# Optimization experiments

Hardware: AMD Instinct MI355X
Metric: run time of the kernel (lower is better)

The kernel has to match this reference:

```python
import jax, jax.numpy as jnp
import numpy as np

D = 1024
H = 16
HD = D // H


def setup_inputs() -> dict:
    key = jax.random.key(0)
    ks = jax.random.split(key, 9)
    s = 1.0 / np.sqrt(D)
    inp = {
        "x": jax.random.normal(ks[0], (2, 2048, D), dtype=jnp.float32),
        "Wq": jax.random.uniform(ks[1], (D, D), jnp.float32, -s, s),
        "bq": jax.random.uniform(ks[2], (D,), jnp.float32, -s, s),
        "Wk": jax.random.uniform(ks[3], (D, D), jnp.float32, -s, s),
        "bk": jax.random.uniform(ks[4], (D,), jnp.float32, -s, s),
        "Wv": jax.random.uniform(ks[5], (D, D), jnp.float32, -s, s),
        "bv": jax.random.uniform(ks[6], (D,), jnp.float32, -s, s),
        "Wo": jax.random.uniform(ks[7], (D, D), jnp.float32, -s, s),
        "bo": jax.random.uniform(ks[8], (D,), jnp.float32, -s, s),
    }
    return inp


def reference(x, Wq, bq, Wk, bk, Wv, bv, Wo, bo):
    B, S, _ = x.shape
    scale = jnp.sqrt(jnp.asarray(HD, dtype=jnp.float32))
    # QKV projections, split into heads: [B, H, S, HD]
    def proj(W, b):
        y = jnp.einsum('bsd,de->bse', x, W) + b
        return y.reshape(B, S, H, HD).transpose(0, 2, 1, 3)
    Q, K, V = proj(Wq, bq), proj(Wk, bk), proj(Wv, bv)
    scores = jnp.einsum('bhqd,bhkd->bhqk', Q, K) / scale  # [B,H,S,S]
    attn = jax.nn.softmax(scores, axis=-1)
    ctx = jnp.einsum('bhqk,bhkd->bhqd', attn, V)
    ctx = ctx.transpose(0, 2, 1, 3).reshape(B, S, D)
    return jnp.einsum('bsd,de->bse', ctx, Wo) + bo
```

## Files before the change

### kernel.cpp

```cpp
#include <hip/hip_runtime.h>
#include <hip/hip_bf16.h>

typedef __attribute__((ext_vector_type(8))) _Float16 f16x8;
typedef __attribute__((ext_vector_type(4))) float f32x4;

constexpr int Sc  = 2048;
constexpr int Dc  = 1024;
constexpr int Hc  = 16;
constexpr int HDc = 64;
constexpr int Mc  = 4096;

constexpr float ECs = 0.18033688011112042f;

__device__ __forceinline__ ushort f2h(float f) {
  return __builtin_bit_cast(ushort, (_Float16)f);
}

union US8 {
  ushort u[8];
  uint   w[4];
  f16x8  v;
};

__global__ __launch_bounds__(256) void split_x_kernel(
    const float* __restrict__ X, ushort* __restrict__ H) {
  const int i    = blockIdx.x * 256 + threadIdx.x;
  const float4 v = ((const float4*)X)[i];
  ushort4 h;
  h.x = f2h(v.x);
  h.y = f2h(v.y);
  h.z = f2h(v.z);
  h.w = f2h(v.w);
  ((ushort4*)H)[i] = h;
}

struct SplitP {
  const float* W[4];
  ushort*      Th[4];
};

__global__ __launch_bounds__(256) void split_wt_kernel(SplitP p) {
  __shared__ float T[64][69];
  const int z = blockIdx.z;
  const float* W = p.W[z];
  const int t  = threadIdx.x;
  const int c  = (t & 15) * 4;
  const int r  = t >> 4;
  const int n0 = blockIdx.x * 64, k0 = blockIdx.y * 64;
#pragma unroll
  for (int pp = 0; pp < 4; ++pp) {
    const int k    = r + pp * 16;
    const float4 v = *(const float4*)(W + (size_t)(k0 + k) * 1024 + n0 + c);
    T[k][c + 0] = v.x;
    T[k][c + 1] = v.y;
    T[k][c + 2] = v.z;
    T[k][c + 3] = v.w;
  }
  __syncthreads();
#pragma unroll
  for (int pp = 0; pp < 4; ++pp) {
    const int n = r + pp * 16;
    ushort4 h;
    h.x = f2h(T[c + 0][n]);
    h.y = f2h(T[c + 1][n]);
    h.z = f2h(T[c + 2][n]);
    h.w = f2h(T[c + 3][n]);
    *(ushort4*)(p.Th[z] + (size_t)(n0 + n) * 1024 + k0 + c) = h;
  }
}

struct GemmP {
  const ushort* Bh[3];
  const float*  bias[3];
  void*         Out[3];
};

template <bool QKV>
__global__ __launch_bounds__(256) void gemm_f16(
    const ushort* __restrict__ A, GemmP p) {
  __shared__ __align__(16) ushort As[128 * 32];
  __shared__ __align__(16) ushort Bs[128 * 32];

  const int t  = threadIdx.x;
  const int z  = blockIdx.z;
  const int m0 = blockIdx.x * 128, n0 = blockIdx.y * 128;
  const ushort* Bh  = p.Bh[z];
  const float* bias = p.bias[z];

  const int lane = t & 63, wave = t >> 6;
  const int wm = (wave & 1) * 64, wn = (wave >> 1) * 64;

  f32x4 acc[4][4];
#pragma unroll
  for (int i = 0; i < 4; ++i)
#pragma unroll
    for (int j = 0; j < 4; ++j) acc[i][j] = (f32x4){0.f, 0.f, 0.f, 0.f};

  const int am = t >> 2;
  const int ac = t & 3;
  const ushort* gA  = A  + (size_t)(m0 + am) * 1024 + ac * 8;
  const ushort* gBh = Bh + (size_t)(n0 + am) * 1024 + ac * 8;
  const int sw = ((ac + (am >> 1)) & 3) * 8;
  const int l0 = am * 32 + sw, l1 = (am + 64) * 32 + sw;

  const int fr  = lane & 15;
  const int fkb = (((lane >> 4) + (fr >> 1)) & 3) * 16;

  f16x8 rA0, rA1, rH0, rH1;
  rA0 = *(const f16x8*)(gA);
  rA1 = *(const f16x8*)(gA + 64 * 1024);
  rH0 = *(const f16x8*)(gBh);
  rH1 = *(const f16x8*)(gBh + 64 * 1024);

  for (int k0 = 0; k0 < 1024; k0 += 32) {
    __syncthreads();
    *(f16x8*)&As[l0] = rA0;
    *(f16x8*)&As[l1] = rA1;
    *(f16x8*)&Bs[l0] = rH0;
    *(f16x8*)&Bs[l1] = rH1;
    __syncthreads();

    if (k0 + 32 < 1024) {
      const int kn = k0 + 32;
      rA0 = *(const f16x8*)(gA + kn);
      rA1 = *(const f16x8*)(gA + kn + 64 * 1024);
      rH0 = *(const f16x8*)(gBh + kn);
      rH1 = *(const f16x8*)(gBh + kn + 64 * 1024);
    }

    f16x8 a[4], b_h[4];
#pragma unroll
    for (int i = 0; i < 4; ++i) {
      const int ra = (wm + i * 16 + fr) * 64 + fkb;
      const int rb = (wn + i * 16 + fr) * 64 + fkb;
      a[i]   = *(const f16x8*)((const char*)As + ra);
      b_h[i] = *(const f16x8*)((const char*)Bs + rb);
    }
#pragma unroll
    for (int i = 0; i < 4; ++i)
#pragma unroll
      for (int j = 0; j < 4; ++j)
        acc[i][j] = __builtin_amdgcn_mfma_f32_16x16x32_f16(a[i], b_h[j], acc[i][j], 0, 0, 0);
  }

  const float osc = (QKV && z == 0) ? ECs : 1.0f;
  const int cr = (lane >> 4) * 4;
  const int cc = lane & 15;
#pragma unroll
  for (int j = 0; j < 4; ++j) {
    const int n    = n0 + wn + j * 16 + cc;
    const float bv = bias[n];
#pragma unroll
    for (int i = 0; i < 4; ++i) {
      const int mb = m0 + wm + i * 16 + cr;
#pragma unroll
      for (int r = 0; r < 4; ++r) {
        const int m   = mb + r;
        const float v = (acc[i][j][r] + bv) * osc;
        if (QKV) {
          const int b = m >> 11, s = m & 2047, h = n >> 6, hd = n & 63;
          ((ushort*)p.Out[z])[(((size_t)(b * Hc + h) * Sc + s) << 6) + hd] = f2h(v);
        } else {
          ((float*)p.Out[z])[(size_t)m * 1024 + n] = v;
        }
      }
    }
  }
}

__global__ __launch_bounds__(256) void attn_mfma3(
    const ushort* __restrict__ Q, const ushort* __restrict__ K,
    const ushort* __restrict__ V, ushort* __restrict__ CTX) {
  __shared__ __align__(16) ushort Ks[64 * 72];
  __shared__ __align__(16) ushort Vt[64 * 72];

  const int t    = threadIdx.x;
  const int lane = t & 63, wave = t >> 6;
  const int c16 = lane & 15, quad = lane >> 4;
  const int bh = blockIdx.x, qt = blockIdx.y;
  const int bb = bh >> 4, hh = bh & 15;

  const ushort* Qb = Q + (size_t)bh * Sc * HDc + (size_t)qt * 128 * HDc;
  const ushort* Kb = K + (size_t)bh * Sc * HDc;
  const ushort* Vb = V + (size_t)bh * Sc * HDc;

  f16x8 aq[2][2];
#pragma unroll
  for (int mt = 0; mt < 2; ++mt)
#pragma unroll
    for (int c = 0; c < 2; ++c)
      aq[mt][c] = *(const f16x8*)(Qb + (size_t)(wave * 32 + mt * 16 + c16) * 64 + c * 32 + quad * 8);

  US8 ones_u;
#pragma unroll
  for (int e = 0; e < 8; ++e) ones_u.u[e] = 0x3C00;
  const f16x8 ones = ones_u.v;

  f32x4 ctx[2][4], lacc[2];
#pragma unroll
  for (int mt = 0; mt < 2; ++mt) {
    lacc[mt] = (f32x4){0.f, 0.f, 0.f, 0.f};
#pragma unroll
    for (int j = 0; j < 4; ++j) ctx[mt][j] = (f32x4){0.f, 0.f, 0.f, 0.f};
  }

  const int krow = t >> 2, kc = (t & 3) * 8;
  const int kg = t & 15, dg = t >> 4;
  const int lb = ((kg >> 3) << 5) | ((kg & 3) << 3) | (((kg >> 2) & 1) << 2);

  const ushort* gK = Kb + (size_t)krow * 64 + kc;
  const ushort* gV = Vb + (size_t)(kg * 4) * 64 + dg * 4;

  f16x8 kr0, kr1;
  ushort4 vr[4];
  kr0 = *(const f16x8*)(gK);
  kr1 = *(const f16x8*)(gK + 32);
#pragma unroll
  for (int i = 0; i < 4; ++i) vr[i] = *(const ushort4*)(gV + (size_t)i * 64);

  for (int kt = 0; kt < 32; ++kt) {
    __syncthreads();
    *(f16x8*)&Ks[krow * 72 + kc]      = kr0;
    *(f16x8*)&Ks[krow * 72 + kc + 32] = kr1;
    {
      const uint* w0 = (const uint*)&vr[0];
      const uint* w1 = (const uint*)&vr[1];
      const uint* w2 = (const uint*)&vr[2];
      const uint* w3 = (const uint*)&vr[3];
#pragma unroll
      for (int j = 0; j < 4; ++j) {
        const int  wd  = j >> 1;
        const uint sel = (j & 1) ? 0x07060302u : 0x05040100u;
        const uint lo  = __builtin_amdgcn_perm(w1[wd], w0[wd], sel);
        const uint hi  = __builtin_amdgcn_perm(w3[wd], w2[wd], sel);
        *(uint2*)&Vt[(dg * 4 + j) * 72 + lb] = make_uint2(lo, hi);
      }
    }
    __syncthreads();

    if (kt < 31) {
      const size_t adv = (size_t)(kt + 1) * 64 * 64;
      kr0 = *(const f16x8*)(gK + adv);
      kr1 = *(const f16x8*)(gK + adv + 32);
#pragma unroll
      for (int i = 0; i < 4; ++i) vr[i] = *(const ushort4*)(gV + adv + (size_t)i * 64);
    }

    f32x4 st[2][4];
#pragma unroll
    for (int mt = 0; mt < 2; ++mt)
#pragma unroll
      for (int j = 0; j < 4; ++j) st[mt][j] = (f32x4){0.f, 0.f, 0.f, 0.f};
#pragma unroll
    for (int c = 0; c < 2; ++c)
#pragma unroll
      for (int j = 0; j < 4; ++j) {
        const f16x8 ak = *(const f16x8*)&Ks[(j * 16 + c16) * 72 + c * 32 + quad * 8];
        st[0][j] = __builtin_amdgcn_mfma_f32_16x16x32_f16(ak, aq[0][c], st[0][j], 0, 0, 0);
        st[1][j] = __builtin_amdgcn_mfma_f32_16x16x32_f16(ak, aq[1][c], st[1][j], 0, 0, 0);
      }

    US8 pf[2][2];
#pragma unroll
    for (int mt = 0; mt < 2; ++mt)
#pragma unroll
      for (int c2 = 0; c2 < 2; ++c2)
#pragma unroll
        for (int w = 0; w < 4; ++w) {
          const int jj = c2 * 2 + (w >> 1);
          const int r0 = (w & 1) * 2;
          const float pe = __builtin_amdgcn_exp2f(st[mt][jj][r0]);
          const float po = __builtin_amdgcn_exp2f(st[mt][jj][r0 + 1]);
          const auto pk = __builtin_amdgcn_cvt_pkrtz(pe, po);
          pf[mt][c2].w[w] = __builtin_bit_cast(uint, pk);
        }

#pragma unroll
    for (int c2 = 0; c2 < 2; ++c2) {
      lacc[0] = __builtin_amdgcn_mfma_f32_16x16x32_f16(pf[0][c2].v, ones, lacc[0], 0, 0, 0);
      lacc[1] = __builtin_amdgcn_mfma_f32_16x16x32_f16(pf[1][c2].v, ones, lacc[1], 0, 0, 0);
#pragma unroll
      for (int j = 0; j < 4; ++j) {
        const f16x8 bv = *(const f16x8*)&Vt[(j * 16 + c16) * 72 + c2 * 32 + quad * 8];
        ctx[0][j] = __builtin_amdgcn_mfma_f32_16x16x32_f16(pf[0][c2].v, bv, ctx[0][j], 0, 0, 0);
        ctx[1][j] = __builtin_amdgcn_mfma_f32_16x16x32_f16(pf[1][c2].v, bv, ctx[1][j], 0, 0, 0);
      }
    }
  }

#pragma unroll
  for (int mt = 0; mt < 2; ++mt) {
#pragma unroll
    for (int r = 0; r < 4; ++r) {
      const float inv = 1.f / lacc[mt][r];
      const int srow  = qt * 128 + wave * 32 + mt * 16 + quad * 4 + r;
      const size_t rb = ((size_t)(bb * Sc + srow)) * 1024 + hh * 64;
#pragma unroll
      for (int j = 0; j < 4; ++j)
        CTX[rb + j * 16 + c16] = f2h(ctx[mt][j][r] * inv);
    }
  }
}

extern "C" void kernel_launch(void* const* d_in, const int* in_sizes, int n_in,
                              void* d_out, int out_size, void* d_ws, size_t ws_size,
                              hipStream_t stream) {
  (void)in_sizes; (void)n_in; (void)out_size; (void)ws_size;
  const float* x  = (const float*)d_in[0];
  const float* Wq = (const float*)d_in[1];
  const float* bq = (const float*)d_in[2];
  const float* Wk = (const float*)d_in[3];
  const float* bk = (const float*)d_in[4];
  const float* Wv = (const float*)d_in[5];
  const float* bv = (const float*)d_in[6];
  const float* Wo = (const float*)d_in[7];
  const float* bo = (const float*)d_in[8];

  const size_t MB = 1024 * 1024;
  char* w    = (char*)d_ws;
  ushort* Qw = (ushort*)(w + 0 * MB);
  ushort* Kw = (ushort*)(w + 8 * MB);
  ushort* Vw = (ushort*)(w + 16 * MB);
  ushort* Cw = (ushort*)(w + 24 * MB);
  ushort* Xh = (ushort*)(w + 32 * MB);
  ushort* WT = (ushort*)(w + 40 * MB);
  ushort* Whq = WT + 0 * 1048576;
  ushort* Whk = WT + 1 * 1048576;
  ushort* Whv = WT + 2 * 1048576;
  ushort* Who = WT + 3 * 1048576;

  const dim3 blk(256);

  split_x_kernel<<<4096, blk, 0, stream>>>(x, Xh);

  SplitP sp;
  sp.W[0] = Wq; sp.W[1] = Wk; sp.W[2] = Wv; sp.W[3] = Wo;
  sp.Th[0] = Whq; sp.Th[1] = Whk; sp.Th[2] = Whv; sp.Th[3] = Who;
  split_wt_kernel<<<dim3(16, 16, 4), blk, 0, stream>>>(sp);

  GemmP pq;
  pq.Bh[0] = Whq; pq.Bh[1] = Whk; pq.Bh[2] = Whv;
  pq.bias[0] = bq; pq.bias[1] = bk; pq.bias[2] = bv;
  pq.Out[0] = Qw; pq.Out[1] = Kw; pq.Out[2] = Vw;
  gemm_f16<true><<<dim3(Mc / 128, Dc / 128, 3), blk, 0, stream>>>(Xh, pq);

  attn_mfma3<<<dim3(2 * Hc, Sc / 128), blk, 0, stream>>>(Qw, Kw, Vw, Cw);

  GemmP po;
  po.Bh[0] = po.Bh[1] = po.Bh[2] = Who;
  po.bias[0] = po.bias[1] = po.bias[2] = bo;
  po.Out[0] = po.Out[1] = po.Out[2] = d_out;
  gemm_f16<false><<<dim3(Mc / 128, Dc / 128, 1), blk, 0, stream>>>(Cw, po);
}
```

Baseline: 199.2 us.

## Split attention key range across two blocks and add a combine kernel

The attention grid gains a z dimension that splits the 2048 keys into two halves. Each block writes an unnormalized fp16 partial context and its row sums to workspace, and a new combine kernel adds the two partials and normalizes them. The goal is to double the block count so the 512-block grid fills the GPU better. The cost is an extra launch, extra global traffic for the partials, and fp16 rounding of the unnormalized sums. The score MFMA chain is also restructured to start from a zero constant instead of zeroing the accumulators.

```diff
diff --git a/kernel.cpp b/kernel.cpp
--- a/kernel.cpp
+++ b/kernel.cpp
@@ -170,19 +170,20 @@
 
 __global__ __launch_bounds__(256) void attn_mfma3(
     const ushort* __restrict__ Q, const ushort* __restrict__ K,
-    const ushort* __restrict__ V, ushort* __restrict__ CTX) {
+    const ushort* __restrict__ V, ushort* __restrict__ CTXP,
+    float* __restrict__ LACC) {
   __shared__ __align__(16) ushort Ks[64 * 72];
   __shared__ __align__(16) ushort Vt[64 * 72];
 
   const int t    = threadIdx.x;
   const int lane = t & 63, wave = t >> 6;
   const int c16 = lane & 15, quad = lane >> 4;
-  const int bh = blockIdx.x, qt = blockIdx.y;
+  const int bh = blockIdx.x, qt = blockIdx.y, z = blockIdx.z;
   const int bb = bh >> 4, hh = bh & 15;
 
   const ushort* Qb = Q + (size_t)bh * Sc * HDc + (size_t)qt * 128 * HDc;
-  const ushort* Kb = K + (size_t)bh * Sc * HDc;
-  const ushort* Vb = V + (size_t)bh * Sc * HDc;
+  const ushort* Kb = K + (size_t)bh * Sc * HDc + (size_t)z * 16 * 64 * HDc;
+  const ushort* Vb = V + (size_t)bh * Sc * HDc + (size_t)z * 16 * 64 * HDc;
 
   f16x8 aq[2][2];
 #pragma unroll
@@ -195,6 +196,7 @@
 #pragma unroll
   for (int e = 0; e < 8; ++e) ones_u.u[e] = 0x3C00;
   const f16x8 ones = ones_u.v;
+  const f32x4 kZ = (f32x4){0.f, 0.f, 0.f, 0.f};
 
   f32x4 ctx[2][4], lacc[2];
 #pragma unroll
@@ -218,7 +220,7 @@
 #pragma unroll
   for (int i = 0; i < 4; ++i) vr[i] = *(const ushort4*)(gV + (size_t)i * 64);
 
-  for (int kt = 0; kt < 32; ++kt) {
+  for (int kt = 0; kt < 16; ++kt) {
     __syncthreads();
     *(f16x8*)&Ks[krow * 72 + kc]      = kr0;
     *(f16x8*)&Ks[krow * 72 + kc + 32] = kr1;
@@ -238,7 +240,7 @@
     }
     __syncthreads();
 
-    if (kt < 31) {
+    if (kt < 15) {
       const size_t adv = (size_t)(kt + 1) * 64 * 64;
       kr0 = *(const f16x8*)(gK + adv);
       kr1 = *(const f16x8*)(gK + adv + 32);
@@ -248,17 +250,17 @@
 
     f32x4 st[2][4];
 #pragma unroll
-    for (int mt = 0; mt < 2; ++mt)
-#pragma unroll
-      for (int j = 0; j < 4; ++j) st[mt][j] = (f32x4){0.f, 0.f, 0.f, 0.f};
-#pragma unroll
-    for (int c = 0; c < 2; ++c)
-#pragma unroll
-      for (int j = 0; j < 4; ++j) {
-        const f16x8 ak = *(const f16x8*)&Ks[(j * 16 + c16) * 72 + c * 32 + quad * 8];
-        st[0][j] = __builtin_amdgcn_mfma_f32_16x16x32_f16(ak, aq[0][c], st[0][j], 0, 0, 0);
-        st[1][j] = __builtin_amdgcn_mfma_f32_16x16x32_f16(ak, aq[1][c], st[1][j], 0, 0, 0);
-      }
+    for (int j = 0; j < 4; ++j) {
+      const f16x8 ak0 = *(const f16x8*)&Ks[(j * 16 + c16) * 72 + quad * 8];
+      st[0][j] = __builtin_amdgcn_mfma_f32_16x16x32_f16(ak0, aq[0][0], kZ, 0, 0, 0);
+      st[1][j] = __builtin_amdgcn_mfma_f32_16x16x32_f16(ak0, aq[1][0], kZ, 0, 0, 0);
+    }
+#pragma unroll
+    for (int j = 0; j < 4; ++j) {
+      const f16x8 ak1 = *(const f16x8*)&Ks[(j * 16 + c16) * 72 + 32 + quad * 8];
+      st[0][j] = __builtin_amdgcn_mfma_f32_16x16x32_f16(ak1, aq[0][1], st[0][j], 0, 0, 0);
+      st[1][j] = __builtin_amdgcn_mfma_f32_16x16x32_f16(ak1, aq[1][1], st[1][j], 0, 0, 0);
+    }
 
     US8 pf[2][2];
 #pragma unroll
@@ -288,18 +290,40 @@
     }
   }
 
+  ushort* Cp = CTXP + (size_t)z * Mc * 1024;
+  float*  Lp = LACC + (size_t)z * 2 * Hc * Sc;
 #pragma unroll
   for (int mt = 0; mt < 2; ++mt) {
 #pragma unroll
     for (int r = 0; r < 4; ++r) {
-      const float inv = 1.f / lacc[mt][r];
       const int srow  = qt * 128 + wave * 32 + mt * 16 + quad * 4 + r;
       const size_t rb = ((size_t)(bb * Sc + srow)) * 1024 + hh * 64;
 #pragma unroll
       for (int j = 0; j < 4; ++j)
-        CTX[rb + j * 16 + c16] = f2h(ctx[mt][j][r] * inv);
-    }
-  }
+        Cp[rb + j * 16 + c16] = f2h(ctx[mt][j][r]);
+      if (c16 == 0) Lp[bh * Sc + srow] = lacc[mt][r];
+    }
+  }
+}
+
+__global__ __launch_bounds__(256) void combine_kernel(
+    const ushort* __restrict__ CTXP, const float* __restrict__ LACC,
+    ushort* __restrict__ Cw) {
+  const int i  = blockIdx.x * 256 + threadIdx.x;
+  const int m  = i >> 7;
+  const int kc = (i & 127) * 8;
+  const int b = m >> 11, s = m & 2047, h = kc >> 6;
+  const int li = (b * Hc + h) * Sc + s;
+  const float l0 = LACC[li];
+  const float l1 = LACC[2 * Hc * Sc + li];
+  const float inv = 1.f / (l0 + l1);
+  US8 c0, c1, o;
+  c0.v = *(const f16x8*)(CTXP + (size_t)m * 1024 + kc);
+  c1.v = *(const f16x8*)(CTXP + (size_t)Mc * 1024 + (size_t)m * 1024 + kc);
+#pragma unroll
+  for (int e = 0; e < 8; ++e)
+    o.u[e] = f2h(((float)c0.v[e] + (float)c1.v[e]) * inv);
+  *(f16x8*)(Cw + (size_t)m * 1024 + kc) = o.v;
 }
 
 extern "C" void kernel_launch(void* const* d_in, const int* in_sizes, int n_in,
@@ -318,16 +342,18 @@
 
   const size_t MB = 1024 * 1024;
   char* w    = (char*)d_ws;
-  ushort* Qw = (ushort*)(w + 0 * MB);
-  ushort* Kw = (ushort*)(w + 8 * MB);
-  ushort* Vw = (ushort*)(w + 16 * MB);
-  ushort* Cw = (ushort*)(w + 24 * MB);
-  ushort* Xh = (ushort*)(w + 32 * MB);
-  ushort* WT = (ushort*)(w + 40 * MB);
+  ushort* Qw  = (ushort*)(w + 0 * MB);
+  ushort* Kw  = (ushort*)(w + 8 * MB);
+  ushort* Vw  = (ushort*)(w + 16 * MB);
+  ushort* Cp  = (ushort*)(w + 24 * MB);
+  ushort* Xh  = (ushort*)(w + 32 * MB);
+  ushort* WT  = (ushort*)(w + 40 * MB);
   ushort* Whq = WT + 0 * 1048576;
   ushort* Whk = WT + 1 * 1048576;
   ushort* Whv = WT + 2 * 1048576;
   ushort* Who = WT + 3 * 1048576;
+  float*  Lp  = (float*)(w + 40 * MB);
+  ushort* Cw  = (ushort*)(w + 48 * MB);
 
   const dim3 blk(256);
 
@@ -344,7 +370,9 @@
   pq.Out[0] = Qw; pq.Out[1] = Kw; pq.Out[2] = Vw;
   gemm_f16<true><<<dim3(Mc / 128, Dc / 128, 3), blk, 0, stream>>>(Xh, pq);
 
-  attn_mfma3<<<dim3(2 * Hc, Sc / 128), blk, 0, stream>>>(Qw, Kw, Vw, Cw);
+  attn_mfma3<<<dim3(2 * Hc, Sc / 128, 2), blk, 0, stream>>>(Qw, Kw, Vw, Cp, Lp);
+
+  combine_kernel<<<Mc * 1024 / 8 / 256, blk, 0, stream>>>(Cp, Lp, Cw);
 
   GemmP po;
   po.Bh[0] = po.Bh[1] = po.Bh[2] = Who;
```

After: 208.8 us. 1.05x slower.
